# Performance work log

Measured on AMD Instinct MI355X. Metric: run time of the kernel, lower is better.

## Reference

```python
import jax, jax.numpy as jnp
import numpy as np

T = 2048          # tokens (flattened batch*seq, vLLM style)
HID = 2048        # hidden_size
NH = 16           # num_heads
D_NOPE = 128
D_ROPE = 64
D_QK = D_NOPE + D_ROPE   # 192
D_V = 128
Q_LORA = 1536
KV_LORA = 512
THETA = 10000.0
EPS = 1e-6
SCALING = D_QK ** -0.5


def _rmsnorm(x, g):
    return x * jax.lax.rsqrt(jnp.mean(x * x, axis=-1, keepdims=True) + EPS) * g


def _rope(pos, x):
    # interleaved (is_neox_style=False) rotary embedding
    d = x.shape[-1]
    inv = 1.0 / (THETA ** (jnp.arange(0, d, 2, dtype=jnp.float32) / d))
    f = pos.astype(jnp.float32)[:, None] * inv          # [T, d/2]
    cos, sin = jnp.cos(f), jnp.sin(f)
    for _ in range(x.ndim - 2):                          # broadcast over heads
        cos, sin = cos[:, None], sin[:, None]
    x1, x2 = x[..., 0::2], x[..., 1::2]
    o1 = x1 * cos - x2 * sin
    o2 = x1 * sin + x2 * cos
    return jnp.stack([o1, o2], axis=-1).reshape(x.shape)


def setup_inputs() -> dict:
    key = jax.random.key(0)
    ks = jax.random.split(key, 6)
    s = 0.02
    return {
        "hidden_states": jax.random.normal(ks[0], (T, HID), jnp.float32),
        "positions": jnp.arange(T, dtype=jnp.int32),
        "w_qkv_a": jax.random.normal(ks[1], (HID, Q_LORA + KV_LORA + D_ROPE), jnp.float32) * s,
        "g_q": jnp.ones((Q_LORA,), jnp.float32),
        "w_q_b": jax.random.normal(ks[2], (Q_LORA, NH * D_QK), jnp.float32) * s,
        "g_kv": jnp.ones((KV_LORA,), jnp.float32),
        "w_kv_b": jax.random.normal(ks[3], (KV_LORA, NH * (D_NOPE + D_V)), jnp.float32) * s,
        "w_o": jax.random.normal(ks[4], (NH * D_V, HID), jnp.float32) * s,
    }


def reference(hidden_states, positions, w_qkv_a, g_q, w_q_b, g_kv, w_kv_b, w_o):
    # fused low-rank a-projection: [T, q_lora + kv_lora + rope]
    qkv_a = hidden_states @ w_qkv_a
    q_lat = qkv_a[:, :Q_LORA]
    kv_lat = qkv_a[:, Q_LORA:Q_LORA + KV_LORA]
    k_pe = qkv_a[:, Q_LORA + KV_LORA:]                   # [T, rope]

    # query path: rmsnorm -> b-projection -> [T, H, d_qk]
    q = (_rmsnorm(q_lat, g_q) @ w_q_b).reshape(T, NH, D_QK)
    q_nope, q_pe = q[..., :D_NOPE], q[..., D_NOPE:]

    # kv path: rmsnorm -> b-projection -> [T, H, nope + v]
    kv = (_rmsnorm(kv_lat, g_kv) @ w_kv_b).reshape(T, NH, D_NOPE + D_V)
    k_nope, v = kv[..., :D_NOPE], kv[..., D_NOPE:]

    q_pe = _rope(positions, q_pe)                        # [T, H, rope]
    k_pe = _rope(positions, k_pe)                        # [T, rope] shared MQA rope key

    qf = jnp.concatenate([q_nope, q_pe], axis=-1)        # [T, H, d_qk]
    kf = jnp.concatenate([k_nope, jnp.broadcast_to(k_pe[:, None, :], (T, NH, D_ROPE))], axis=-1)

    scores = jnp.einsum("thd,shd->hts", qf, kf) * SCALING   # [H, T, T]
    mask = jnp.tril(jnp.ones((T, T), dtype=bool))
    scores = jnp.where(mask, scores, jnp.finfo(scores.dtype).min)
    probs = jax.nn.softmax(scores, axis=-1)
    out = jnp.einsum("hts,shd->thd", probs, v)           # [T, H, d_v]
    return out.reshape(T, NH * D_V) @ w_o                # [T, hidden]
```

## Files before the change

kernel.cpp:

```cpp
#include <hip/hip_runtime.h>
#include <hip/hip_bf16.h>
#include <math.h>

typedef __bf16 bf16_t;
typedef __bf16 bf16x8 __attribute__((ext_vector_type(8)));
typedef float floatx4 __attribute__((ext_vector_type(4)));
typedef int intx4 __attribute__((ext_vector_type(4)));

#define T_TOK 2048
#define HID 2048
#define NH 16
#define D_NOPE 128
#define D_ROPE 64
#define D_QK 192
#define D_V 128
#define Q_LORA 1536
#define KV_LORA 512
#define QKV_N 2112
#define QKV_NPAD 2176
#define SCALING 0.07216878364870323f
#define LOG2E 1.442695041f
#define EXP_C1 (SCALING * LOG2E)
#define EXP_C2 (12.0f * LOG2E)

#define MFMA_BF16(a, b, c) __builtin_amdgcn_mfma_f32_16x16x32_bf16(a, b, c, 0, 0, 0)

__device__ __forceinline__ void gload16(const void* g, void* l) {
    __builtin_amdgcn_global_load_lds(
        (const __attribute__((address_space(1))) unsigned int*)g,
        (__attribute__((address_space(3))) unsigned int*)l, 16, 0, 0);
}

template <int MODE>
__device__ __forceinline__ void gemm_body(
    const bf16_t* __restrict__ A, const bf16_t* __restrict__ Bt,
    float* __restrict__ Cf, bf16_t* __restrict__ Cb,
    bf16_t* __restrict__ kfull, bf16_t* __restrict__ vtmp,
    int N, int K, int m0, int n0, bf16_t* As, bf16_t* Bs)
{
    const int tid = threadIdx.x;
    const int lane = tid & 63;
    const int w = tid >> 6;
    const int wm = w >> 1, wn = w & 1;
    const int l15 = lane & 15, quad = lane >> 4;
    const int ckey = (l15 >> 1) & 3;

    floatx4 acc[4][4] = {};

#define GSTAGE(db_, k0_)                                                                 \
    do {                                                                                 \
        _Pragma("unroll")                                                                \
        for (int it = 0; it < 4; ++it) {                                                 \
            int slot = it * 256 + tid;                                                   \
            int kk2 = slot >> 9;                                                         \
            int r = (slot >> 2) & 127;                                                   \
            int c = slot & 3;                                                            \
            int cs = c ^ ((r >> 1) & 3);                                                 \
            gload16((const char*)(A + (size_t)(m0 + r) * K + (k0_) + kk2 * 32 + cs * 8), \
                    (char*)(As + (size_t)(db_)*8192) + slot * 16);                       \
            gload16((const char*)(Bt + (size_t)(n0 + r) * K + (k0_) + kk2 * 32 + cs * 8),\
                    (char*)(Bs + (size_t)(db_)*8192) + slot * 16);                       \
        }                                                                                \
    } while (0)

    GSTAGE(0, 0);
    int db = 0;
    for (int k0 = 0; k0 < K; k0 += 64) {
        __syncthreads();
        if (k0 + 64 < K) GSTAGE(db ^ 1, k0 + 64);
        const bf16_t* Ab = As + (size_t)db * 8192;
        const bf16_t* Bb = Bs + (size_t)db * 8192;
#pragma unroll
        for (int kk2 = 0; kk2 < 2; ++kk2) {
            bf16x8 af[4], bfr[4];
#pragma unroll
            for (int mi = 0; mi < 4; ++mi)
                af[mi] = *(const bf16x8*)(Ab + kk2 * 4096 +
                                          (wm * 64 + mi * 16 + l15) * 32 +
                                          (quad ^ ckey) * 8);
#pragma unroll
            for (int ni = 0; ni < 4; ++ni)
                bfr[ni] = *(const bf16x8*)(Bb + kk2 * 4096 +
                                           (wn * 64 + ni * 16 + l15) * 32 +
                                           (quad ^ ckey) * 8);
#pragma unroll
            for (int mi = 0; mi < 4; ++mi)
#pragma unroll
                for (int ni = 0; ni < 4; ++ni)
                    acc[mi][ni] = MFMA_BF16(af[mi], bfr[ni], acc[mi][ni]);
        }
        db ^= 1;
    }
#undef GSTAGE

#pragma unroll
    for (int mi = 0; mi < 4; ++mi)
#pragma unroll
        for (int ni = 0; ni < 4; ++ni)
#pragma unroll
            for (int r = 0; r < 4; ++r) {
                int row = m0 + wm * 64 + mi * 16 + quad * 4 + r;
                int col = n0 + wn * 64 + ni * 16 + l15;
                float v = acc[mi][ni][r];
                if (MODE == 1) {
                    Cb[(size_t)row * N + col] = (bf16_t)v;
                } else if (MODE == 2) {
                    int h = col >> 8, dd = col & 255;
                    if (dd < 128)
                        kfull[((size_t)h * T_TOK + row) * 192 + dd] = (bf16_t)v;
                    else
                        vtmp[(size_t)row * 2048 + h * 128 + (dd - 128)] = (bf16_t)v;
                } else {
                    Cf[(size_t)row * N + col] = v;
                }
            }
}

template <int MODE>
__global__ __launch_bounds__(256) void gemm_mfma(
    const bf16_t* __restrict__ A, const bf16_t* __restrict__ Bt,
    float* __restrict__ Cf, bf16_t* __restrict__ Cb,
    bf16_t* __restrict__ kfull, bf16_t* __restrict__ vtmp,
    int M, int N, int K)
{
    __shared__ __align__(16) bf16_t As[2 * 8192];
    __shared__ __align__(16) bf16_t Bs[2 * 8192];
    gemm_body<MODE>(A, Bt, Cf, Cb, kfull, vtmp, N, K,
                    blockIdx.y * 128, blockIdx.x * 128, As, Bs);
}

__global__ __launch_bounds__(256) void gemm_dual(
    const bf16_t* __restrict__ qn, const bf16_t* __restrict__ wqb,
    bf16_t* __restrict__ qbuf,
    const bf16_t* __restrict__ kvn, const bf16_t* __restrict__ wkvb,
    bf16_t* __restrict__ kfull, bf16_t* __restrict__ vtmp)
{
    __shared__ __align__(16) bf16_t As[2 * 8192];
    __shared__ __align__(16) bf16_t Bs[2 * 8192];
    int id = blockIdx.x;
    if (id < 384) {
        gemm_body<1>(qn, wqb, nullptr, qbuf, nullptr, nullptr,
                     3072, Q_LORA, (id / 24) * 128, (id % 24) * 128, As, Bs);
    } else {
        int i2 = id - 384;
        gemm_body<2>(kvn, wkvb, nullptr, nullptr, kfull, vtmp,
                     4096, KV_LORA, (i2 / 32) * 128, (i2 % 32) * 128, As, Bs);
    }
}

__global__ void transpose_all(const float* __restrict__ w0, const float* __restrict__ w1,
                              const float* __restrict__ w2, const float* __restrict__ w3,
                              bf16_t* __restrict__ o0, bf16_t* __restrict__ o1,
                              bf16_t* __restrict__ o2, bf16_t* __restrict__ o3) {
    const float* in; bf16_t* out; int K, N;
    switch (blockIdx.z) {
        case 0: in = w0; out = o0; K = 2048; N = 2112; break;
        case 1: in = w1; out = o1; K = 1536; N = 3072; break;
        case 2: in = w2; out = o2; K = 512;  N = 4096; break;
        default: in = w3; out = o3; K = 2048; N = 2048; break;
    }
    int n0 = blockIdx.x * 32, k0 = blockIdx.y * 32;
    if (n0 >= N || k0 >= K) return;
    __shared__ float tile[32][33];
    int tx = threadIdx.x, ty = threadIdx.y;
    for (int i = ty; i < 32; i += 8)
        tile[i][tx] = in[(size_t)(k0 + i) * N + n0 + tx];
    __syncthreads();
    for (int i = ty; i < 32; i += 8)
        out[(size_t)(n0 + i) * K + k0 + tx] = (bf16_t)tile[tx][i];
}

__global__ void transpose_b2b(const bf16_t* __restrict__ in, bf16_t* __restrict__ out,
                              int R, int C) {
    __shared__ bf16_t tile[32][33];
    int c0 = blockIdx.x * 32, r0 = blockIdx.y * 32;
    int tx = threadIdx.x, ty = threadIdx.y;
    for (int i = ty; i < 32; i += 8)
        tile[i][tx] = in[(size_t)(r0 + i) * C + c0 + tx];
    __syncthreads();
    for (int i = ty; i < 32; i += 8)
        out[(size_t)(c0 + i) * R + r0 + tx] = tile[tx][i];
}

__global__ void cvt_f2b(const float* __restrict__ in, bf16_t* __restrict__ out, int n) {
    int i = blockIdx.x * 256 + threadIdx.x;
    if (i < n) out[i] = (bf16_t)in[i];
}

__global__ void mid_fuse(const float* __restrict__ qkv_a, const int* __restrict__ pos,
                         const float* __restrict__ g_q, const float* __restrict__ g_kv,
                         bf16_t* __restrict__ qn, bf16_t* __restrict__ kvn,
                         bf16_t* __restrict__ kfull) {
    int t = blockIdx.x, tid = threadIdx.x;
    const float* x = qkv_a + (size_t)t * QKV_NPAD;
    __shared__ float red[256];
    float ss = 0.f;
    for (int c = tid; c < Q_LORA; c += 256) { float v = x[c]; ss += v * v; }
    red[tid] = ss;
    __syncthreads();
    for (int o = 128; o > 0; o >>= 1) {
        if (tid < o) red[tid] += red[tid + o];
        __syncthreads();
    }
    float rq = rsqrtf(red[0] / (float)Q_LORA + 1e-6f);
    __syncthreads();
    ss = 0.f;
    for (int c = Q_LORA + tid; c < Q_LORA + KV_LORA; c += 256) { float v = x[c]; ss += v * v; }
    red[tid] = ss;
    __syncthreads();
    for (int o = 128; o > 0; o >>= 1) {
        if (tid < o) red[tid] += red[tid + o];
        __syncthreads();
    }
    float rkv = rsqrtf(red[0] / (float)KV_LORA + 1e-6f);

    for (int c = tid; c < Q_LORA; c += 256)
        qn[(size_t)t * Q_LORA + c] = (bf16_t)(x[c] * rq * g_q[c]);
    for (int c = tid; c < KV_LORA; c += 256)
        kvn[(size_t)t * KV_LORA + c] = (bf16_t)(x[Q_LORA + c] * rkv * g_kv[c]);

    if (tid < 32) {
        int i = tid;
        double inv = pow(10000.0, -(double)(2 * i) / 64.0);
        double fd = (double)pos[t] * inv;
        float c = (float)cos(fd), s = (float)sin(fd);
        float x1 = x[Q_LORA + KV_LORA + 2 * i], x2 = x[Q_LORA + KV_LORA + 2 * i + 1];
        bf16_t v0 = (bf16_t)(x1 * c - x2 * s);
        bf16_t v1 = (bf16_t)(x1 * s + x2 * c);
#pragma unroll
        for (int h = 0; h < NH; ++h) {
            kfull[((size_t)h * T_TOK + t) * 192 + 128 + 2 * i] = v0;
            kfull[((size_t)h * T_TOK + t) * 192 + 128 + 2 * i + 1] = v1;
        }
    }
}

__global__ void rope_q_kernel(bf16_t* __restrict__ q, const int* __restrict__ pos) {
    int idx = blockIdx.x * blockDim.x + threadIdx.x;
    if (idx >= T_TOK * NH * 32) return;
    int i = idx & 31;
    int h = (idx >> 5) & (NH - 1);
    int t = idx >> 9;
    double inv = pow(10000.0, -(double)(2 * i) / 64.0);
    double fd = (double)pos[t] * inv;
    float c = (float)cos(fd), s = (float)sin(fd);
    bf16_t* base = q + (size_t)t * (NH * D_QK) + h * D_QK + D_NOPE;
    float x1 = (float)base[2 * i], x2 = (float)base[2 * i + 1];
    base[2 * i] = (bf16_t)(x1 * c - x2 * s);
    base[2 * i + 1] = (bf16_t)(x1 * s + x2 * c);
}

__global__ __launch_bounds__(256, 2) void attn_part(
    const bf16_t* __restrict__ qbuf, const bf16_t* __restrict__ kfull,
    const bf16_t* __restrict__ vT,
    bf16_t* __restrict__ oP0, bf16_t* __restrict__ oP1, float* __restrict__ l_part)
{
    const int id = blockIdx.x;
    const int h = id & 15;
    const int c = (id >> 4) & 3;
    const int qt = 15 - (id >> 6);
    const int q0 = qt * 128;
    const int nTile = 2 * (qt + 1);
    const int tbase = nTile >> 2, trem = nTile & 3;
    const int sz = tbase + (c < trem ? 1 : 0);
    const int sBeg = c * tbase + (c < trem ? c : trem);
    const int sEnd = sBeg + sz;
    const int unit = qt * 16 + h;
    const int tid = threadIdx.x, lane = tid & 63, w = tid >> 6;
    const int l15 = lane & 15, quad = lane >> 4;
    const int ckey = (l15 >> 1) & 3;

    __shared__ __align__(16) bf16_t kn2[2][6 * 64 * 32];
    __shared__ __align__(16) bf16_t vt2[2 * 128 * 32];
    __shared__ __align__(16) bf16_t p_s[128 * 64];

    bf16x8 qf[2][6];
#pragma unroll
    for (int st = 0; st < 2; ++st) {
        const bf16_t* qp = qbuf + (size_t)(q0 + w * 32 + st * 16 + l15) * (NH * D_QK) +
                           h * D_QK;
#pragma unroll
        for (int kk = 0; kk < 6; ++kk)
            qf[st][kk] = *(const bf16x8*)(qp + kk * 32 + quad * 8);
    }

    bf16x8 ones;
#pragma unroll
    for (int j = 0; j < 8; ++j) ones[j] = (bf16_t)1.0f;

    floatx4 o[2][8] = {};
    floatx4 lac[2] = {};
    intx4 vreg[4];

#define STAGE_KN(buf_, s0_)                                                              \
    do {                                                                                 \
        _Pragma("unroll")                                                                \
        for (int it = 0; it < 6; ++it) {                                                 \
            int slot = it * 256 + tid;                                                   \
            int kk = slot >> 8, s = (slot >> 2) & 63, cc = slot & 3;                     \
            int cs = cc ^ ((s >> 1) & 3);                                                \
            gload16((const char*)(kfull + ((size_t)h * T_TOK + (s0_) + s) * 192 +        \
                                  kk * 32 + cs * 8),                                     \
                    (char*)kn2[buf_] + slot * 16);                                       \
        }                                                                                \
    } while (0)

#define VLOAD(s0_)                                                                       \
    do {                                                                                 \
        _Pragma("unroll")                                                                \
        for (int it = 0; it < 4; ++it) {                                                 \
            int slot = it * 256 + tid;                                                   \
            int ks = slot >> 9, d = (slot >> 2) & 127, cc = slot & 3;                    \
            vreg[it] = *(const intx4*)(vT + ((size_t)h * 128 + d) * T_TOK + (s0_) +      \
                                       ks * 32 + cc * 8);                                \
        }                                                                                \
    } while (0)

#define VWRITE()                                                                         \
    do {                                                                                 \
        _Pragma("unroll")                                                                \
        for (int it = 0; it < 4; ++it) {                                                 \
            int slot = it * 256 + tid;                                                   \
            int ks = slot >> 9, d = (slot >> 2) & 127, cc = slot & 3;                    \
            *(intx4*)((char*)vt2 +                                                       \
                      (size_t)((ks * 512 + d * 4 + (cc ^ ((d >> 1) & 3))) * 16)) =       \
                vreg[it];                                                                \
        }                                                                                \
    } while (0)

    if (sz > 0) {
        VLOAD(sBeg * 64);
        STAGE_KN(0, sBeg * 64);
        VWRITE();
    }

    for (int si = sBeg; si < sEnd; ++si) {
        const int s0 = si * 64;
        const int buf = (si - sBeg) & 1;
        __syncthreads();
        if (si + 1 < sEnd) {
            VLOAD(s0 + 64);
            STAGE_KN(buf ^ 1, s0 + 64);
        }

        floatx4 s_acc[2][4] = {};
        __builtin_amdgcn_s_setprio(1);
#pragma unroll
        for (int ni = 0; ni < 4; ++ni) {
#pragma unroll
            for (int kk = 0; kk < 6; ++kk) {
                bf16x8 b = *(const bf16x8*)(kn2[buf] + kk * 2048 +
                                            (ni * 16 + l15) * 32 + (quad ^ ckey) * 8);
                s_acc[0][ni] = MFMA_BF16(qf[0][kk], b, s_acc[0][ni]);
                s_acc[1][ni] = MFMA_BF16(qf[1][kk], b, s_acc[1][ni]);
            }
        }
        __builtin_amdgcn_s_setprio(0);

        const bool diag = (si >= 2 * qt);
#pragma unroll
        for (int st = 0; st < 2; ++st)
#pragma unroll
            for (int ni = 0; ni < 4; ++ni)
#pragma unroll
                for (int r = 0; r < 4; ++r) {
                    int prow = w * 32 + st * 16 + quad * 4 + r;
                    int pcol = ni * 16 + l15;
                    float pv = exp2f(s_acc[st][ni][r] * EXP_C1 - EXP_C2);
                    if (diag && (s0 + pcol) > (q0 + prow)) pv = 0.f;
                    p_s[prow * 64 + ((((pcol >> 3) ^ (prow & 7))) << 3) + (pcol & 7)] =
                        (bf16_t)pv;
                }

        __builtin_amdgcn_s_setprio(1);
#pragma unroll
        for (int ks = 0; ks < 2; ++ks) {
            bf16x8 a0, a1;
            {
                int arow = w * 32 + l15;
                a0 = *(const bf16x8*)(p_s + arow * 64 +
                                      (((ks * 4 + quad) ^ (arow & 7)) << 3));
                arow += 16;
                a1 = *(const bf16x8*)(p_s + arow * 64 +
                                      (((ks * 4 + quad) ^ (arow & 7)) << 3));
            }
            lac[0] = MFMA_BF16(a0, ones, lac[0]);
            lac[1] = MFMA_BF16(a1, ones, lac[1]);
#pragma unroll
            for (int ni = 0; ni < 8; ++ni) {
                bf16x8 b = *(const bf16x8*)(vt2 + ks * 4096 +
                                            (ni * 16 + l15) * 32 + (quad ^ ckey) * 8);
                o[0][ni] = MFMA_BF16(a0, b, o[0][ni]);
                o[1][ni] = MFMA_BF16(a1, b, o[1][ni]);
            }
        }
        __builtin_amdgcn_s_setprio(0);

        __syncthreads();
        if (si + 1 < sEnd) VWRITE();
    }

    bf16_t* op = ((c < 2) ? oP0 : oP1) + (size_t)(unit * 2 + (c & 1)) * 128 * 128;
#pragma unroll
    for (int st = 0; st < 2; ++st) {
#pragma unroll
        for (int ni = 0; ni < 8; ++ni)
#pragma unroll
            for (int r = 0; r < 4; ++r) {
                int lrow = w * 32 + st * 16 + quad * 4 + r;
                op[(size_t)lrow * 128 + ni * 16 + l15] = (bf16_t)o[st][ni][r];
            }
        if (l15 == 0)
#pragma unroll
            for (int r = 0; r < 4; ++r) {
                int lrow = w * 32 + st * 16 + quad * 4 + r;
                l_part[((size_t)unit * 4 + c) * 128 + lrow] = lac[st][r];
            }
    }
#undef STAGE_KN
#undef VLOAD
#undef VWRITE
}

__global__ void attn_combine(const bf16_t* __restrict__ oP0,
                             const bf16_t* __restrict__ oP1,
                             const float* __restrict__ l_part,
                             bf16_t* __restrict__ attn_o)
{
    int idx = blockIdx.x * 256 + threadIdx.x;
    int t = idx >> 8, cg = idx & 255;
    int col = cg * 8;
    int h = col >> 7, d = col & 127;
    int qt = t >> 7, lrow = t & 127;
    size_t unit = (size_t)qt * 16 + h;
    const float* lp = l_part + unit * 4 * 128 + lrow;
    float inv = 1.f / (lp[0] + lp[128] + lp[256] + lp[384]);
    size_t r0 = ((unit * 2 + 0) * 128 + lrow) * 128 + d;
    size_t r1 = ((unit * 2 + 1) * 128 + lrow) * 128 + d;
    bf16x8 a0 = *(const bf16x8*)(oP0 + r0);
    bf16x8 a1 = *(const bf16x8*)(oP0 + r1);
    bf16x8 a2 = *(const bf16x8*)(oP1 + r0);
    bf16x8 a3 = *(const bf16x8*)(oP1 + r1);
    bf16x8 out;
#pragma unroll
    for (int j = 0; j < 8; ++j)
        out[j] = (bf16_t)(((float)a0[j] + (float)a1[j] + (float)a2[j] + (float)a3[j]) * inv);
    *(bf16x8*)(attn_o + (size_t)t * (NH * D_V) + col) = out;
}

extern "C" void kernel_launch(void* const* d_in, const int* in_sizes, int n_in,
                              void* d_out, int out_size, void* d_ws, size_t ws_size,
                              hipStream_t stream) {
    const float* hidden = (const float*)d_in[0];
    const int* positions = (const int*)d_in[1];
    const float* w_qkv_a = (const float*)d_in[2];
    const float* g_q = (const float*)d_in[3];
    const float* w_q_b = (const float*)d_in[4];
    const float* g_kv = (const float*)d_in[5];
    const float* w_kv_b = (const float*)d_in[6];
    const float* w_o = (const float*)d_in[7];
    float* out = (float*)d_out;

    char* p = (char*)d_ws;
    float* qkv_a = (float*)p;
    bf16_t* attn_o = (bf16_t*)p;
    p += (size_t)T_TOK * QKV_NPAD * 4;
    bf16_t* hbf = (bf16_t*)p;
    bf16_t* qn = hbf;
    bf16_t* kvn = hbf + (size_t)T_TOK * Q_LORA;
    p += (size_t)T_TOK * HID * 2;
    bf16_t* qbuf = (bf16_t*)p;  p += (size_t)T_TOK * NH * D_QK * 2;
    bf16_t* vtmp = (bf16_t*)p;  p += (size_t)T_TOK * NH * D_V * 2;
    bf16_t* kfull = (bf16_t*)p; p += (size_t)NH * T_TOK * 192 * 2;
    bf16_t* vT = (bf16_t*)p;    p += (size_t)NH * 128 * T_TOK * 2;
    bf16_t* wt_qkv_a = (bf16_t*)p; p += (size_t)QKV_NPAD * HID * 2;
    bf16_t* wt_q_b = (bf16_t*)p;   p += (size_t)3072 * Q_LORA * 2;
    bf16_t* wt_kv_b = (bf16_t*)p;  p += (size_t)4096 * KV_LORA * 2;
    bf16_t* wt_o = (bf16_t*)p;

    bf16_t* oP0 = wt_qkv_a;
    bf16_t* oP1 = (bf16_t*)((char*)d_ws + (size_t)T_TOK * HID * 2);
    float* l_part = (float*)vtmp;

    dim3 tb(32, 8);

    cvt_f2b<<<(T_TOK * HID) / 256, 256, 0, stream>>>(hidden, hbf, T_TOK * HID);
    transpose_all<<<dim3(128, 64, 4), tb, 0, stream>>>(
        w_qkv_a, w_q_b, w_kv_b, w_o, wt_qkv_a, wt_q_b, wt_kv_b, wt_o);

    gemm_mfma<0><<<dim3(QKV_NPAD / 128, T_TOK / 128), 256, 0, stream>>>(
        hbf, wt_qkv_a, qkv_a, nullptr, nullptr, nullptr, T_TOK, QKV_NPAD, HID);

    mid_fuse<<<T_TOK, 256, 0, stream>>>(qkv_a, positions, g_q, g_kv, qn, kvn, kfull);

    gemm_dual<<<896, 256, 0, stream>>>(qn, wt_q_b, qbuf, kvn, wt_kv_b, kfull, vtmp);
    rope_q_kernel<<<(T_TOK * NH * 32) / 256, 256, 0, stream>>>(qbuf, positions);
    transpose_b2b<<<dim3(HID / 32, T_TOK / 32), tb, 0, stream>>>(vtmp, vT, T_TOK, HID);

    attn_part<<<1024, 256, 0, stream>>>(qbuf, kfull, vT, oP0, oP1, l_part);
    attn_combine<<<(T_TOK * 256) / 256, 256, 0, stream>>>(oP0, oP1, l_part, attn_o);

    gemm_mfma<0><<<dim3(HID / 128, T_TOK / 128), 256, 0, stream>>>(
        attn_o, wt_o, out, nullptr, nullptr, nullptr, T_TOK, HID, NH * D_V);
}
```

Before: 346.5 us.

## Fuse V transpose, q rope, and hidden conversion into neighboring kernels

The kv b-projection epilogue now writes V directly in transposed layout through an LDS staging tile, which removes the separate bf16 transpose kernel. Query rope moves into the attention kernel's Q fragment load, using a cos/sin table computed in mid_fuse, so the standalone rope pass over qbuf goes away. The fp32-to-bf16 conversion of hidden states is folded into the weight transpose launch as an extra grid slice. The goal is fewer launches and fewer global round trips, at the cost of more epilogue work and shared memory traffic in the GEMM.

```diff
diff --git a/kernel.cpp b/kernel.cpp
--- a/kernel.cpp
+++ b/kernel.cpp
@@ -35,9 +35,11 @@
 __device__ __forceinline__ void gemm_body(
     const bf16_t* __restrict__ A, const bf16_t* __restrict__ Bt,
     float* __restrict__ Cf, bf16_t* __restrict__ Cb,
-    bf16_t* __restrict__ kfull, bf16_t* __restrict__ vtmp,
-    int N, int K, int m0, int n0, bf16_t* As, bf16_t* Bs)
+    bf16_t* __restrict__ kfull, bf16_t* __restrict__ vT,
+    int N, int K, int m0, int n0, bf16_t* S)
 {
+    bf16_t* As = S;
+    bf16_t* Bs = S + 16384;
     const int tid = threadIdx.x;
     const int lane = tid & 63;
     const int w = tid >> 6;
@@ -93,6 +95,44 @@
     }
 #undef GSTAGE
 
+    if (MODE == 2) {
+        const int hh = n0 >> 8;
+        if ((n0 & 255) == 0) {
+#pragma unroll
+            for (int mi = 0; mi < 4; ++mi)
+#pragma unroll
+                for (int ni = 0; ni < 4; ++ni)
+#pragma unroll
+                    for (int r = 0; r < 4; ++r) {
+                        int row = m0 + wm * 64 + mi * 16 + quad * 4 + r;
+                        int dd = wn * 64 + ni * 16 + l15;
+                        kfull[((size_t)hh * T_TOK + row) * 192 + dd] =
+                            (bf16_t)acc[mi][ni][r];
+                    }
+        } else {
+            __syncthreads();
+            bf16_t* Tq = S;
+#pragma unroll
+            for (int mi = 0; mi < 4; ++mi)
+#pragma unroll
+                for (int ni = 0; ni < 4; ++ni)
+#pragma unroll
+                    for (int r = 0; r < 4; ++r) {
+                        int rloc = wm * 64 + mi * 16 + quad * 4 + r;
+                        int cloc = wn * 64 + ni * 16 + l15;
+                        Tq[cloc * 136 + rloc] = (bf16_t)acc[mi][ni][r];
+                    }
+            __syncthreads();
+#pragma unroll
+            for (int pass = 0; pass < 8; ++pass) {
+                int dcol = pass * 16 + w * 4 + quad;
+                bf16x8 vv = *(const bf16x8*)(Tq + dcol * 136 + l15 * 8);
+                *(bf16x8*)(vT + ((size_t)hh * 128 + dcol) * T_TOK + m0 + l15 * 8) = vv;
+            }
+        }
+        return;
+    }
+
 #pragma unroll
     for (int mi = 0; mi < 4; ++mi)
 #pragma unroll
@@ -104,12 +144,6 @@
                 float v = acc[mi][ni][r];
                 if (MODE == 1) {
                     Cb[(size_t)row * N + col] = (bf16_t)v;
-                } else if (MODE == 2) {
-                    int h = col >> 8, dd = col & 255;
-                    if (dd < 128)
-                        kfull[((size_t)h * T_TOK + row) * 192 + dd] = (bf16_t)v;
-                    else
-                        vtmp[(size_t)row * 2048 + h * 128 + (dd - 128)] = (bf16_t)v;
                 } else {
                     Cf[(size_t)row * N + col] = v;
                 }
@@ -120,38 +154,47 @@
 __global__ __launch_bounds__(256) void gemm_mfma(
     const bf16_t* __restrict__ A, const bf16_t* __restrict__ Bt,
     float* __restrict__ Cf, bf16_t* __restrict__ Cb,
-    bf16_t* __restrict__ kfull, bf16_t* __restrict__ vtmp,
+    bf16_t* __restrict__ kfull, bf16_t* __restrict__ vT,
     int M, int N, int K)
 {
-    __shared__ __align__(16) bf16_t As[2 * 8192];
-    __shared__ __align__(16) bf16_t Bs[2 * 8192];
-    gemm_body<MODE>(A, Bt, Cf, Cb, kfull, vtmp, N, K,
-                    blockIdx.y * 128, blockIdx.x * 128, As, Bs);
+    __shared__ __align__(16) bf16_t S[4 * 8192];
+    gemm_body<MODE>(A, Bt, Cf, Cb, kfull, vT, N, K,
+                    blockIdx.y * 128, blockIdx.x * 128, S);
 }
 
 __global__ __launch_bounds__(256) void gemm_dual(
     const bf16_t* __restrict__ qn, const bf16_t* __restrict__ wqb,
     bf16_t* __restrict__ qbuf,
     const bf16_t* __restrict__ kvn, const bf16_t* __restrict__ wkvb,
-    bf16_t* __restrict__ kfull, bf16_t* __restrict__ vtmp)
+    bf16_t* __restrict__ kfull, bf16_t* __restrict__ vT)
 {
-    __shared__ __align__(16) bf16_t As[2 * 8192];
-    __shared__ __align__(16) bf16_t Bs[2 * 8192];
+    __shared__ __align__(16) bf16_t S[4 * 8192];
     int id = blockIdx.x;
     if (id < 384) {
         gemm_body<1>(qn, wqb, nullptr, qbuf, nullptr, nullptr,
-                     3072, Q_LORA, (id / 24) * 128, (id % 24) * 128, As, Bs);
+                     3072, Q_LORA, (id / 24) * 128, (id % 24) * 128, S);
     } else {
         int i2 = id - 384;
-        gemm_body<2>(kvn, wkvb, nullptr, nullptr, kfull, vtmp,
-                     4096, KV_LORA, (i2 / 32) * 128, (i2 % 32) * 128, As, Bs);
+        gemm_body<2>(kvn, wkvb, nullptr, nullptr, kfull, vT,
+                     4096, KV_LORA, (i2 / 32) * 128, (i2 % 32) * 128, S);
     }
 }
 
 __global__ void transpose_all(const float* __restrict__ w0, const float* __restrict__ w1,
                               const float* __restrict__ w2, const float* __restrict__ w3,
+                              const float* __restrict__ hidden,
                               bf16_t* __restrict__ o0, bf16_t* __restrict__ o1,
-                              bf16_t* __restrict__ o2, bf16_t* __restrict__ o3) {
+                              bf16_t* __restrict__ o2, bf16_t* __restrict__ o3,
+                              bf16_t* __restrict__ hbf) {
+    int n0 = blockIdx.x * 32, k0 = blockIdx.y * 32;
+    int tx = threadIdx.x, ty = threadIdx.y;
+    if (blockIdx.z == 4) {
+        if (n0 >= 2048 || k0 >= 2048) return;
+        for (int i = ty; i < 32; i += 8)
+            hbf[(size_t)(k0 + i) * 2048 + n0 + tx] =
+                (bf16_t)hidden[(size_t)(k0 + i) * 2048 + n0 + tx];
+        return;
+    }
     const float* in; bf16_t* out; int K, N;
     switch (blockIdx.z) {
         case 0: in = w0; out = o0; K = 2048; N = 2112; break;
@@ -159,10 +202,8 @@
         case 2: in = w2; out = o2; K = 512;  N = 4096; break;
         default: in = w3; out = o3; K = 2048; N = 2048; break;
     }
-    int n0 = blockIdx.x * 32, k0 = blockIdx.y * 32;
     if (n0 >= N || k0 >= K) return;
     __shared__ float tile[32][33];
-    int tx = threadIdx.x, ty = threadIdx.y;
     for (int i = ty; i < 32; i += 8)
         tile[i][tx] = in[(size_t)(k0 + i) * N + n0 + tx];
     __syncthreads();
@@ -170,27 +211,10 @@
         out[(size_t)(n0 + i) * K + k0 + tx] = (bf16_t)tile[tx][i];
 }
 
-__global__ void transpose_b2b(const bf16_t* __restrict__ in, bf16_t* __restrict__ out,
-                              int R, int C) {
-    __shared__ bf16_t tile[32][33];
-    int c0 = blockIdx.x * 32, r0 = blockIdx.y * 32;
-    int tx = threadIdx.x, ty = threadIdx.y;
-    for (int i = ty; i < 32; i += 8)
-        tile[i][tx] = in[(size_t)(r0 + i) * C + c0 + tx];
-    __syncthreads();
-    for (int i = ty; i < 32; i += 8)
-        out[(size_t)(c0 + i) * R + r0 + tx] = tile[tx][i];
-}
-
-__global__ void cvt_f2b(const float* __restrict__ in, bf16_t* __restrict__ out, int n) {
-    int i = blockIdx.x * 256 + threadIdx.x;
-    if (i < n) out[i] = (bf16_t)in[i];
-}
-
 __global__ void mid_fuse(const float* __restrict__ qkv_a, const int* __restrict__ pos,
                          const float* __restrict__ g_q, const float* __restrict__ g_kv,
                          bf16_t* __restrict__ qn, bf16_t* __restrict__ kvn,
-                         bf16_t* __restrict__ kfull) {
+                         bf16_t* __restrict__ kfull, float2* __restrict__ ropet) {
     int t = blockIdx.x, tid = threadIdx.x;
     const float* x = qkv_a + (size_t)t * QKV_NPAD;
     __shared__ float red[256];
@@ -224,6 +248,7 @@
         double inv = pow(10000.0, -(double)(2 * i) / 64.0);
         double fd = (double)pos[t] * inv;
         float c = (float)cos(fd), s = (float)sin(fd);
+        ropet[t * 32 + i] = make_float2(c, s);
         float x1 = x[Q_LORA + KV_LORA + 2 * i], x2 = x[Q_LORA + KV_LORA + 2 * i + 1];
         bf16_t v0 = (bf16_t)(x1 * c - x2 * s);
         bf16_t v1 = (bf16_t)(x1 * s + x2 * c);
@@ -235,24 +260,9 @@
     }
 }
 
-__global__ void rope_q_kernel(bf16_t* __restrict__ q, const int* __restrict__ pos) {
-    int idx = blockIdx.x * blockDim.x + threadIdx.x;
-    if (idx >= T_TOK * NH * 32) return;
-    int i = idx & 31;
-    int h = (idx >> 5) & (NH - 1);
-    int t = idx >> 9;
-    double inv = pow(10000.0, -(double)(2 * i) / 64.0);
-    double fd = (double)pos[t] * inv;
-    float c = (float)cos(fd), s = (float)sin(fd);
-    bf16_t* base = q + (size_t)t * (NH * D_QK) + h * D_QK + D_NOPE;
-    float x1 = (float)base[2 * i], x2 = (float)base[2 * i + 1];
-    base[2 * i] = (bf16_t)(x1 * c - x2 * s);
-    base[2 * i + 1] = (bf16_t)(x1 * s + x2 * c);
-}
-
 __global__ __launch_bounds__(256, 2) void attn_part(
     const bf16_t* __restrict__ qbuf, const bf16_t* __restrict__ kfull,
-    const bf16_t* __restrict__ vT,
+    const bf16_t* __restrict__ vT, const float2* __restrict__ ropet,
     bf16_t* __restrict__ oP0, bf16_t* __restrict__ oP1, float* __restrict__ l_part)
 {
     const int id = blockIdx.x;
@@ -282,6 +292,19 @@
 #pragma unroll
         for (int kk = 0; kk < 6; ++kk)
             qf[st][kk] = *(const bf16x8*)(qp + kk * 32 + quad * 8);
+    }
+#pragma unroll
+    for (int st = 0; st < 2; ++st) {
+        int t = q0 + w * 32 + st * 16 + l15;
+#pragma unroll
+        for (int kk = 4; kk < 6; ++kk)
+#pragma unroll
+            for (int p = 0; p < 4; ++p) {
+                float2 cs = ropet[t * 32 + (kk - 4) * 16 + quad * 4 + p];
+                float x1 = (float)qf[st][kk][2 * p], x2 = (float)qf[st][kk][2 * p + 1];
+                qf[st][kk][2 * p] = (bf16_t)(x1 * cs.x - x2 * cs.y);
+                qf[st][kk][2 * p + 1] = (bf16_t)(x1 * cs.y + x2 * cs.x);
+            }
     }
 
     bf16x8 ones;
@@ -478,26 +501,25 @@
     bf16_t* wt_kv_b = (bf16_t*)p;  p += (size_t)4096 * KV_LORA * 2;
     bf16_t* wt_o = (bf16_t*)p;
 
+    float2* ropet = (float2*)vtmp;
+    float* l_part = (float*)((char*)vtmp + (1 << 20));
     bf16_t* oP0 = wt_qkv_a;
     bf16_t* oP1 = (bf16_t*)((char*)d_ws + (size_t)T_TOK * HID * 2);
-    float* l_part = (float*)vtmp;
 
     dim3 tb(32, 8);
 
-    cvt_f2b<<<(T_TOK * HID) / 256, 256, 0, stream>>>(hidden, hbf, T_TOK * HID);
-    transpose_all<<<dim3(128, 64, 4), tb, 0, stream>>>(
-        w_qkv_a, w_q_b, w_kv_b, w_o, wt_qkv_a, wt_q_b, wt_kv_b, wt_o);
+    transpose_all<<<dim3(128, 64, 5), tb, 0, stream>>>(
+        w_qkv_a, w_q_b, w_kv_b, w_o, hidden, wt_qkv_a, wt_q_b, wt_kv_b, wt_o, hbf);
 
     gemm_mfma<0><<<dim3(QKV_NPAD / 128, T_TOK / 128), 256, 0, stream>>>(
         hbf, wt_qkv_a, qkv_a, nullptr, nullptr, nullptr, T_TOK, QKV_NPAD, HID);
 
-    mid_fuse<<<T_TOK, 256, 0, stream>>>(qkv_a, positions, g_q, g_kv, qn, kvn, kfull);
-
-    gemm_dual<<<896, 256, 0, stream>>>(qn, wt_q_b, qbuf, kvn, wt_kv_b, kfull, vtmp);
-    rope_q_kernel<<<(T_TOK * NH * 32) / 256, 256, 0, stream>>>(qbuf, positions);
-    transpose_b2b<<<dim3(HID / 32, T_TOK / 32), tb, 0, stream>>>(vtmp, vT, T_TOK, HID);
-
-    attn_part<<<1024, 256, 0, stream>>>(qbuf, kfull, vT, oP0, oP1, l_part);
+    mid_fuse<<<T_TOK, 256, 0, stream>>>(qkv_a, positions, g_q, g_kv, qn, kvn,
+                                        kfull, ropet);
+
+    gemm_dual<<<896, 256, 0, stream>>>(qn, wt_q_b, qbuf, kvn, wt_kv_b, kfull, vT);
+
+    attn_part<<<1024, 256, 0, stream>>>(qbuf, kfull, vT, ropet, oP0, oP1, l_part);
     attn_combine<<<(T_TOK * 256) / 256, 256, 0, stream>>>(oP0, oP1, l_part, attn_o);
 
     gemm_mfma<0><<<dim3(HID / 128, T_TOK / 128), 256, 0, stream>>>(
```

Result: faster. 302.7 us (-12.6%).
